# Performance work log

Hardware: AMD Instinct MI355X
Metric: run time of the kernel (lower is better)

The kernel has to match this reference:

```python
import jax, jax.numpy as jnp
import numpy as np

B, T, C = 2, 2048, 1024
NH = 16
HD = C // NH

def setup_inputs() -> dict:
    key = jax.random.key(0)
    k1, k2, k3 = jax.random.split(key, 3)
    x = jax.random.normal(k1, (B, T, C), dtype=jnp.float32)
    w_attn = jax.random.normal(k2, (C, 3 * C), dtype=jnp.float32) * 0.02
    w_proj = jax.random.normal(k3, (C, C), dtype=jnp.float32) * 0.02
    return {"x": x, "w_attn": w_attn, "w_proj": w_proj}

def reference(x, w_attn, w_proj):
    b, t, c = x.shape
    qkv = x @ w_attn                                  # [B,T,3C]
    q, k, v = jnp.split(qkv, 3, axis=-1)
    # [B,NH,T,HD]
    q = q.reshape(b, t, NH, HD).transpose(0, 2, 1, 3)
    k = k.reshape(b, t, NH, HD).transpose(0, 2, 1, 3)
    v = v.reshape(b, t, NH, HD).transpose(0, 2, 1, 3)
    scale = 1.0 / np.sqrt(HD).astype(np.float32)
    att = jnp.einsum('bhqd,bhkd->bhqk', q, k) * scale  # [B,NH,T,T]
    causal = jnp.tril(jnp.ones((t, t), dtype=bool))
    att = jnp.where(causal[None, None], att, jnp.float32(-jnp.inf))
    att = jax.nn.softmax(att, axis=-1)
    y = jnp.einsum('bhqk,bhkd->bhqd', att, v)          # [B,NH,T,HD]
    y = y.transpose(0, 2, 1, 3).reshape(b, t, c)
    return y @ w_proj
```

## Files before the change

kernel.cpp:

```cpp
#include <hip/hip_runtime.h>
#include <hip/hip_bf16.h>

#define BB 2
#define TT 2048
#define CCH 1024
#define NHH 16
#define HDD 64
#define M_TOK (BB*TT)
#define N_QKV (3*CCH)

typedef __attribute__((ext_vector_type(8))) short bf16x8;
typedef __attribute__((ext_vector_type(4))) float f32x4;
typedef unsigned short u16;
typedef unsigned int u32;

__device__ __forceinline__ u16 f2bf(float f) {
    union { float f; u32 u; } v; v.f = f;
    u32 u = v.u;
    u32 r = (u + 0x7FFFu + ((u >> 16) & 1u)) >> 16;
    return (u16)r;
}

__device__ __forceinline__ u32 pk_bf16(float a, float b) {
    u32 ua = __float_as_uint(a) + 0x8000u;
    u32 ub = __float_as_uint(b) + 0x8000u;
    return __builtin_amdgcn_perm(ub, ua, 0x07060302u);
}

__device__ __forceinline__ void async_copy16(const void* g, void* l) {
    __builtin_amdgcn_global_load_lds((__attribute__((address_space(1))) void*)g,
                                     (__attribute__((address_space(3))) void*)l,
                                     16, 0, 0);
}


__global__ __launch_bounds__(256) void cast_bf16_kernel(
    const float* __restrict__ src, u16* __restrict__ dst, int n4) {
    int i = blockIdx.x * 256 + threadIdx.x;
    if (i < n4) {
        float4 f = ((const float4*)src)[i];
        ushort4 o;
        o.x = f2bf(f.x); o.y = f2bf(f.y); o.z = f2bf(f.z); o.w = f2bf(f.w);
        ((ushort4*)dst)[i] = o;
    }
}

__global__ __launch_bounds__(256) void transpose_bf16_kernel(
    const float* __restrict__ src, u16* __restrict__ dst, int R, int Cn,
    int scale_rows, float sc) {
    __shared__ float tile[32][33];
    int c0 = blockIdx.x * 32, r0 = blockIdx.y * 32;
    int tx = threadIdx.x, ty = threadIdx.y;
#pragma unroll
    for (int i = ty; i < 32; i += 8)
        tile[i][tx] = src[(size_t)(r0 + i) * Cn + c0 + tx];
    __syncthreads();
#pragma unroll
    for (int i = ty; i < 32; i += 8) {
        float v = tile[tx][i];
        if (c0 + i < scale_rows) v *= sc;
        dst[(size_t)(c0 + i) * R + r0 + tx] = f2bf(v);
    }
}


template<int SWAP, int NJ>
__device__ __forceinline__ void gemm_kloop64(
    const u16* __restrict__ A, const u16* __restrict__ Bt, int K,
    int m0, int n0, int t, u16* __restrict__ As, u16* __restrict__ Bs,
    f32x4 (&acc)[4][4])
{
    int lane = t & 63, w = t >> 6;
    int mw = (w >> 1) * 64, nw = (w & 1) * (NJ * 16);
    int mr = lane & 15, quad = lane >> 4;
    int lr = lane >> 3;
    int cswz = (lane & 7) ^ lr;

    const u16* gA[4]; u16* lA[4];
#pragma unroll
    for (int p = 0; p < 4; ++p) {
        int grp = w * 4 + p;
        gA[p] = A + (size_t)(m0 + grp * 8 + lr) * K + cswz * 8;
        lA[p] = As + ((size_t)grp * 64 + lane) * 8;
    }
    const u16* gB[4]; u16* lB[4];
#pragma unroll
    for (int p = 0; p < NJ; ++p) {
        int grp = w * NJ + p;
        gB[p] = Bt + (size_t)(n0 + grp * 8 + lr) * K + cswz * 8;
        lB[p] = Bs + ((size_t)grp * 64 + lane) * 8;
    }

    int swm = mr & 7;
    for (int k0 = 0; k0 < K; k0 += 64) {
#pragma unroll
        for (int p = 0; p < 4; ++p) async_copy16(gA[p] + k0, lA[p]);
#pragma unroll
        for (int p = 0; p < NJ; ++p) async_copy16(gB[p] + k0, lB[p]);
        __syncthreads();
#pragma unroll
        for (int kk = 0; kk < 2; ++kk) {
            bf16x8 af[4], bfr[4];
#pragma unroll
            for (int i = 0; i < 4; ++i) {
                int r = mw + i * 16 + mr;
                af[i] = *(const bf16x8*)&As[r * 64 + (((kk * 4 + quad) ^ swm) << 3)];
            }
#pragma unroll
            for (int j = 0; j < NJ; ++j) {
                int r = nw + j * 16 + mr;
                bfr[j] = *(const bf16x8*)&Bs[r * 64 + (((kk * 4 + quad) ^ swm) << 3)];
            }
#pragma unroll
            for (int i = 0; i < 4; ++i)
#pragma unroll
                for (int j = 0; j < NJ; ++j) {
                    if (SWAP)
                        acc[i][j] = __builtin_amdgcn_mfma_f32_16x16x32_bf16(bfr[j], af[i], acc[i][j], 0, 0, 0);
                    else
                        acc[i][j] = __builtin_amdgcn_mfma_f32_16x16x32_bf16(af[i], bfr[j], acc[i][j], 0, 0, 0);
                }
        }
        __syncthreads();
    }
}


__global__ __launch_bounds__(256, 3) void qkv_gemm_kernel(
    const u16* __restrict__ A, const u16* __restrict__ Bt,
    u16* __restrict__ Qo, u16* __restrict__ Ko, u16* __restrict__ Vto)
{
    __shared__ u16 As[128 * 64];
    __shared__ u16 Bs[128 * 64];
    int t = threadIdx.x;
    int m0 = blockIdx.y * 128, n0 = blockIdx.x * 128;
    int part = n0 >> 10;
    int lane = t & 63, w = t >> 6;
    int mw = (w >> 1) * 64, nw = (w & 1) * 64;
    int mr = lane & 15, quad = lane >> 4;

    f32x4 zero = {0.f, 0.f, 0.f, 0.f};
    f32x4 acc[4][4];
#pragma unroll
    for (int i = 0; i < 4; ++i)
#pragma unroll
        for (int j = 0; j < 4; ++j) acc[i][j] = zero;

    if (part < 2) {
        gemm_kloop64<1, 4>(A, Bt, CCH, m0, n0, t, As, Bs, acc);
        u16* dstp = part ? Ko : Qo;
#pragma unroll
        for (int i = 0; i < 4; ++i)
#pragma unroll
            for (int j = 0; j < 4; ++j) {
                int tok = m0 + mw + i * 16 + mr;
                int cg0 = n0 + nw + j * 16 + quad * 4;
                int cc = cg0 & 1023;
                int h = cc >> 6, d0 = cc & 63;
                int b = tok >> 11, tt = tok & 2047;
                int bh = b * NHH + h;
                uint2 o;
                o.x = pk_bf16(acc[i][j][0], acc[i][j][1]);
                o.y = pk_bf16(acc[i][j][2], acc[i][j][3]);
                *(uint2*)&dstp[((size_t)bh * TT + tt) * HDD + d0] = o;
            }
    } else {
        gemm_kloop64<0, 4>(A, Bt, CCH, m0, n0, t, As, Bs, acc);
#pragma unroll
        for (int i = 0; i < 4; ++i)
#pragma unroll
            for (int j = 0; j < 4; ++j) {
                int t0 = m0 + mw + i * 16 + quad * 4;
                int cg = n0 + nw + j * 16 + mr;
                int cc = cg & 1023;
                int h = cc >> 6, d = cc & 63;
                int b = t0 >> 11, tt0 = t0 & 2047;
                int bh = b * NHH + h;
                uint2 o;
                o.x = pk_bf16(acc[i][j][0], acc[i][j][1]);
                o.y = pk_bf16(acc[i][j][2], acc[i][j][3]);
                *(uint2*)&Vto[((size_t)bh * HDD + d) * TT + tt0] = o;
            }
    }
}


__global__ __launch_bounds__(256) void proj_gemm_kernel(
    const u16* __restrict__ A, const u16* __restrict__ Bt, float* __restrict__ Cout)
{
    __shared__ u16 As[128 * 64];
    __shared__ u16 Bs[64 * 64];
    int t = threadIdx.x;
    int m0 = blockIdx.y * 128, n0 = blockIdx.x * 64;
    int lane = t & 63, w = t >> 6;
    int mw = (w >> 1) * 64, nw = (w & 1) * 32;
    int mr = lane & 15, quad = lane >> 4;

    f32x4 zero = {0.f, 0.f, 0.f, 0.f};
    f32x4 acc[4][4];
#pragma unroll
    for (int i = 0; i < 4; ++i)
#pragma unroll
        for (int j = 0; j < 4; ++j) acc[i][j] = zero;

    gemm_kloop64<1, 2>(A, Bt, CCH, m0, n0, t, As, Bs, acc);

#pragma unroll
    for (int i = 0; i < 4; ++i)
#pragma unroll
        for (int j = 0; j < 2; ++j) {
            int tok = m0 + mw + i * 16 + mr;
            int cg0 = n0 + nw + j * 16 + quad * 4;
            float4 v;
            v.x = acc[i][j][0]; v.y = acc[i][j][1];
            v.z = acc[i][j][2]; v.w = acc[i][j][3];
            *(float4*)&Cout[(size_t)tok * CCH + cg0] = v;
        }
}


#define PST2 40

template<bool MASK>
__device__ __forceinline__ void tile3(
    const u16* __restrict__ Kb, const u16* __restrict__ Vb, u16* __restrict__ pb,
    bf16x8 qf0, bf16x8 qf1, bf16x8 ones, int m, int quad, int sw, int kh,
    int kvb, int qcol, f32x4 (&o)[4], f32x4& lacc)
{
    f32x4 zero = {0.f, 0.f, 0.f, 0.f};
#pragma unroll
    for (int kc = 0; kc < 2; ++kc) {
        int rr = kh * 32 + kc * 16 + m;
        bf16x8 kf0 = *(const bf16x8*)&Kb[rr * 64 + ((quad ^ sw) << 3)];
        bf16x8 kf1 = *(const bf16x8*)&Kb[rr * 64 + (((quad + 4) ^ sw) << 3)];
        f32x4 s  = __builtin_amdgcn_mfma_f32_16x16x32_bf16(kf0, qf0, zero, 0, 0, 0);
        f32x4 st = __builtin_amdgcn_mfma_f32_16x16x32_bf16(kf1, qf1, s, 0, 0, 0);
        float e0, e1, e2, e3;
#pragma unroll
        for (int r = 0; r < 4; ++r) {
            float v = st[r];
            if (MASK && (kvb + kc * 16 + quad * 4 + r > qcol)) v = -1e30f;
            float e = __builtin_amdgcn_exp2f(v);
            if (r == 0) e0 = e; else if (r == 1) e1 = e; else if (r == 2) e2 = e; else e3 = e;
        }
        uint2 pk; pk.x = pk_bf16(e0, e1); pk.y = pk_bf16(e2, e3);
        *(uint2*)&pb[m * PST2 + kc * 16 + quad * 4] = pk;
    }
    bf16x8 pf = *(const bf16x8*)&pb[m * PST2 + quad * 8];
    lacc = __builtin_amdgcn_mfma_f32_16x16x32_bf16(ones, pf, lacc, 0, 0, 0);
#pragma unroll
    for (int dg = 0; dg < 4; ++dg) {
        int rr = dg * 16 + m;
        bf16x8 vf = *(const bf16x8*)&Vb[rr * 64 + (((kh * 4 + quad) ^ sw) << 3)];
        o[dg] = __builtin_amdgcn_mfma_f32_16x16x32_bf16(vf, pf, o[dg], 0, 0, 0);
    }
}

#define SM_U16 26880

__global__ __launch_bounds__(512, 2) void attn_kernel(
    const u16* __restrict__ Q, const u16* __restrict__ K,
    const u16* __restrict__ Vt, u16* __restrict__ Y)
{
    __shared__ __align__(16) u16 smem[SM_U16];
    int t = threadIdx.x;
    int w = t >> 6, lane = t & 63;
    int m = lane & 15, quad = lane >> 4;
    int iq = w >> 1, kh = w & 1;

    int bid = blockIdx.x;
    int head = bid & 31;
    int g = bid >> 5;
    int pr = (g < 8) ? g : 23 - g;
    int qbA = pr;
    int qbB = 31 - pr;
    int rbA = qbA * 64 + iq * 16;
    int rbB = qbB * 64 + iq * 16;

    const u16* qpA = Q + ((size_t)head * TT + rbA + m) * HDD + quad * 8;
    const u16* qpB = Q + ((size_t)head * TT + rbB + m) * HDD + quad * 8;
    bf16x8 qA0 = *(const bf16x8*)qpA;
    bf16x8 qA1 = *(const bf16x8*)(qpA + 32);
    bf16x8 qB0 = *(const bf16x8*)qpB;
    bf16x8 qB1 = *(const bf16x8*)(qpB + 32);

    bf16x8 ones;
#pragma unroll
    for (int i = 0; i < 8; ++i) ones[i] = (short)0x3F80;

    const u16* kbase = K + (size_t)head * TT * HDD;
    const u16* vbase = Vt + (size_t)head * HDD * TT;
    u16* pbA = smem + 16384 + (w * 2 + 0) * (16 * PST2);
    u16* pbB = smem + 16384 + (w * 2 + 1) * (16 * PST2);

    int lr = lane >> 3;
    int cg = (lane & 7) ^ lr;
    int r0 = w * 8 + lr;
    int loff = (w * 64 + lane) * 8;

    f32x4 zero = {0.f, 0.f, 0.f, 0.f};
    f32x4 oA[4], oB[4], laA = zero, laB = zero;
#pragma unroll
    for (int dg = 0; dg < 4; ++dg) { oA[dg] = zero; oB[dg] = zero; }
    int qcA = rbA + m, qcB = rbB + m;
    int sw = m & 7;

    async_copy16(kbase + (size_t)r0 * 64 + cg * 8, smem + loff);
    async_copy16(vbase + (size_t)r0 * TT + cg * 8, smem + 8192 + loff);

    for (int ic = 0; ic <= qbB; ++ic) {
        int buf = ic & 1;
        int kv0 = ic << 6;
        __syncthreads();
        if (ic < qbB) {
            int nkv = kv0 + 64;
            u16* dK = smem + (buf ^ 1) * 4096;
            u16* dV = smem + 8192 + (buf ^ 1) * 4096;
            async_copy16(kbase + (size_t)(nkv + r0) * 64 + cg * 8, dK + loff);
            async_copy16(vbase + (size_t)r0 * TT + nkv + cg * 8, dV + loff);
        }
        const u16* Kb = smem + buf * 4096;
        const u16* Vb = smem + 8192 + buf * 4096;
        int kvb = kv0 + kh * 32;
        if (ic < qbA)
            tile3<false>(Kb, Vb, pbA, qA0, qA1, ones, m, quad, sw, kh, kvb, qcA, oA, laA);
        else if (ic == qbA)
            tile3<true >(Kb, Vb, pbA, qA0, qA1, ones, m, quad, sw, kh, kvb, qcA, oA, laA);
        if (ic < qbB)
            tile3<false>(Kb, Vb, pbB, qB0, qB1, ones, m, quad, sw, kh, kvb, qcB, oB, laB);
        else
            tile3<true >(Kb, Vb, pbB, qB0, qB1, ones, m, quad, sw, kh, kvb, qcB, oB, laB);
    }

    float lA = laA[0];
    float lB = laB[0];

    __syncthreads();
    f32x4* ob = (f32x4*)smem;
    float* lb = (float*)&smem[26624];
    if (kh) {
        f32x4* dst = ob + (size_t)iq * 512 + lane;
#pragma unroll
        for (int dg = 0; dg < 4; ++dg) {
            dst[dg * 64] = oA[dg];
            dst[(4 + dg) * 64] = oB[dg];
        }
        if (quad == 0) {
            lb[(iq * 2 + 0) * 16 + m] = lA;
            lb[(iq * 2 + 1) * 16 + m] = lB;
        }
    }
    __syncthreads();
    if (!kh) {
        f32x4* src = ob + (size_t)iq * 512 + lane;
#pragma unroll
        for (int dg = 0; dg < 4; ++dg) {
            oA[dg] += src[dg * 64];
            oB[dg] += src[(4 + dg) * 64];
        }
        lA += lb[(iq * 2 + 0) * 16 + m];
        lB += lb[(iq * 2 + 1) * 16 + m];
        float invA = 1.0f / lA, invB = 1.0f / lB;

        int b = head >> 4, h = head & 15;
        size_t roA = ((size_t)(b * TT + rbA + m)) * CCH + h * HDD;
        size_t roB = ((size_t)(b * TT + rbB + m)) * CCH + h * HDD;
#pragma unroll
        for (int dg = 0; dg < 4; ++dg) {
            uint2 ov;
            ov.x = pk_bf16(oA[dg][0] * invA, oA[dg][1] * invA);
            ov.y = pk_bf16(oA[dg][2] * invA, oA[dg][3] * invA);
            *(uint2*)&Y[roA + dg * 16 + quad * 4] = ov;
            ov.x = pk_bf16(oB[dg][0] * invB, oB[dg][1] * invB);
            ov.y = pk_bf16(oB[dg][2] * invB, oB[dg][3] * invB);
            *(uint2*)&Y[roB + dg * 16 + quad * 4] = ov;
        }
    }
}


extern "C" void kernel_launch(void* const* d_in, const int* in_sizes, int n_in,
                              void* d_out, int out_size, void* d_ws, size_t ws_size,
                              hipStream_t stream) {
    const float* x      = (const float*)d_in[0];
    const float* w_attn = (const float*)d_in[1];
    const float* w_proj = (const float*)d_in[2];
    float* out = (float*)d_out;

    char* ws = (char*)d_ws;
    u16* x_bf   = (u16*)ws; ws += (size_t)M_TOK * CCH * 2;
    u16* wqkvT  = (u16*)ws; ws += (size_t)N_QKV * CCH * 2;
    u16* wprojT = (u16*)ws; ws += (size_t)CCH * CCH * 2;
    u16* qbuf   = (u16*)ws; ws += (size_t)BB * NHH * TT * HDD * 2;
    u16* kbuf   = (u16*)ws; ws += (size_t)BB * NHH * TT * HDD * 2;
    u16* vtb    = (u16*)ws; ws += (size_t)BB * NHH * HDD * TT * 2;
    u16* yb     = (u16*)ws; ws += (size_t)M_TOK * CCH * 2;

    const float QSC = 0.125f * 1.44269504088896f;

    cast_bf16_kernel<<<dim3(M_TOK * CCH / 4 / 256), dim3(256), 0, stream>>>(x, x_bf, M_TOK * CCH / 4);
    transpose_bf16_kernel<<<dim3(N_QKV / 32, CCH / 32), dim3(32, 8), 0, stream>>>(
        w_attn, wqkvT, CCH, N_QKV, CCH, QSC);
    transpose_bf16_kernel<<<dim3(CCH / 32, CCH / 32), dim3(32, 8), 0, stream>>>(
        w_proj, wprojT, CCH, CCH, 0, 1.0f);
    qkv_gemm_kernel<<<dim3(24, 32), dim3(256), 0, stream>>>(
        x_bf, wqkvT, qbuf, kbuf, vtb);
    attn_kernel<<<dim3(512), dim3(512), 0, stream>>>(qbuf, kbuf, vtb, yb);
    proj_gemm_kernel<<<dim3(16, 32), dim3(256), 0, stream>>>(yb, wprojT, out);
}
```

Measured before the change: 174.8 us.

## Rewrite QKV GEMM with 256x192 tiles and double-buffered async LDS pipeline

The QKV projection GEMM moves from 128x128 tiles with 256 threads to 256x192 tiles with 512 threads. Loads now go through a two-stage double-buffered async global-to-LDS pipeline with explicit waitcnt and barrier control, and the k-step is split in two halves so the next stage can be issued mid-iteration. The goal is to hide memory latency and cut redundant operand traffic through more reuse per block. In exchange, the grid shrinks to 256 blocks at one block per CU. The V-transpose epilogue now writes single scalar bf16 values with strided addressing, which may coalesce poorly.

```diff
diff --git a/kernel.cpp b/kernel.cpp
--- a/kernel.cpp
+++ b/kernel.cpp
@@ -126,62 +126,122 @@
 }
 
 
-__global__ __launch_bounds__(256, 3) void qkv_gemm_kernel(
+#define QKV_NK 16
+#define QKV_AS_HALF 16384
+#define QKV_BS_HALF 12288
+#define QKV_SMEM_BYTES ((2*QKV_AS_HALF + 2*QKV_BS_HALF) * 2)
+
+__global__ __launch_bounds__(512, 1) void qkv_gemm_kernel(
     const u16* __restrict__ A, const u16* __restrict__ Bt,
     u16* __restrict__ Qo, u16* __restrict__ Ko, u16* __restrict__ Vto)
 {
-    __shared__ u16 As[128 * 64];
-    __shared__ u16 Bs[128 * 64];
+    extern __shared__ __align__(16) u16 smem[];
+    u16* AsB = smem;
+    u16* BsB = smem + 2 * QKV_AS_HALF;
     int t = threadIdx.x;
-    int m0 = blockIdx.y * 128, n0 = blockIdx.x * 128;
-    int part = n0 >> 10;
     int lane = t & 63, w = t >> 6;
-    int mw = (w >> 1) * 64, nw = (w & 1) * 64;
-    int mr = lane & 15, quad = lane >> 4;
+    int m0 = blockIdx.y * 256, n0 = blockIdx.x * 192;
+    int mw = (w >> 1) * 64, nw = (w & 1) * 96;
+    int mr = lane & 15, quad = lane >> 4, swm = mr & 7;
 
     f32x4 zero = {0.f, 0.f, 0.f, 0.f};
-    f32x4 acc[4][4];
+    f32x4 acc[4][6];
 #pragma unroll
     for (int i = 0; i < 4; ++i)
 #pragma unroll
-        for (int j = 0; j < 4; ++j) acc[i][j] = zero;
-
-    if (part < 2) {
-        gemm_kloop64<1, 4>(A, Bt, CCH, m0, n0, t, As, Bs, acc);
-        u16* dstp = part ? Ko : Qo;
+        for (int j = 0; j < 6; ++j) acc[i][j] = zero;
+
+    int lr = lane >> 3;
+    int cswz = (lane & 7) ^ lr;
+    const u16* gA[4]; int lAo[4];
+#pragma unroll
+    for (int p = 0; p < 4; ++p) {
+        int grp = w * 4 + p;
+        gA[p] = A + (size_t)(m0 + grp * 8 + lr) * CCH + cswz * 8;
+        lAo[p] = (grp * 64 + lane) * 8;
+    }
+    const u16* gB[3]; int lBo[3];
+#pragma unroll
+    for (int p = 0; p < 3; ++p) {
+        int grp = w * 3 + p;
+        gB[p] = Bt + (size_t)(n0 + grp * 8 + lr) * CCH + cswz * 8;
+        lBo[p] = (grp * 64 + lane) * 8;
+    }
+
+#define QKV_STAGE(K0, BUF) do {                                               \
+    u16* dA_ = AsB + (BUF) * QKV_AS_HALF;                                     \
+    u16* dB_ = BsB + (BUF) * QKV_BS_HALF;                                     \
+    _Pragma("unroll") for (int p_ = 0; p_ < 4; ++p_)                          \
+        async_copy16(gA[p_] + (K0), dA_ + lAo[p_]);                           \
+    _Pragma("unroll") for (int p_ = 0; p_ < 3; ++p_)                          \
+        async_copy16(gB[p_] + (K0), dB_ + lBo[p_]);                           \
+  } while (0)
+
+    QKV_STAGE(0, 0);
+    QKV_STAGE(64, 1);
+
+    for (int k = 0; k < QKV_NK; ++k) {
+        int cur = k & 1;
+        if (k == QKV_NK - 1) asm volatile("s_waitcnt vmcnt(0)" ::: "memory");
+        else                 asm volatile("s_waitcnt vmcnt(7)" ::: "memory");
+        __builtin_amdgcn_s_barrier();
+        asm volatile("" ::: "memory");
+        const u16* Ac = AsB + cur * QKV_AS_HALF;
+        const u16* Bc = BsB + cur * QKV_BS_HALF;
+        bf16x8 a0[4], a1[4], b0[6], b1[6];
+#pragma unroll
+        for (int i = 0; i < 4; ++i) {
+            int r = (mw + i * 16 + mr) * 64;
+            a0[i] = *(const bf16x8*)&Ac[r + ((quad ^ swm) << 3)];
+            a1[i] = *(const bf16x8*)&Ac[r + (((quad + 4) ^ swm) << 3)];
+        }
+#pragma unroll
+        for (int j = 0; j < 6; ++j) {
+            int r = (nw + j * 16 + mr) * 64;
+            b0[j] = *(const bf16x8*)&Bc[r + ((quad ^ swm) << 3)];
+            b1[j] = *(const bf16x8*)&Bc[r + (((quad + 4) ^ swm) << 3)];
+        }
 #pragma unroll
         for (int i = 0; i < 4; ++i)
 #pragma unroll
-            for (int j = 0; j < 4; ++j) {
-                int tok = m0 + mw + i * 16 + mr;
-                int cg0 = n0 + nw + j * 16 + quad * 4;
-                int cc = cg0 & 1023;
-                int h = cc >> 6, d0 = cc & 63;
-                int b = tok >> 11, tt = tok & 2047;
-                int bh = b * NHH + h;
+            for (int j = 0; j < 6; ++j)
+                acc[i][j] = __builtin_amdgcn_mfma_f32_16x16x32_bf16(b0[j], a0[i], acc[i][j], 0, 0, 0);
+        asm volatile("s_waitcnt lgkmcnt(0)" ::: "memory");
+        __builtin_amdgcn_sched_barrier(0);
+        __builtin_amdgcn_s_barrier();
+        asm volatile("" ::: "memory");
+        if (k < QKV_NK - 2) QKV_STAGE((k + 2) * 64, cur);
+#pragma unroll
+        for (int i = 0; i < 4; ++i)
+#pragma unroll
+            for (int j = 0; j < 6; ++j)
+                acc[i][j] = __builtin_amdgcn_mfma_f32_16x16x32_bf16(b1[j], a1[i], acc[i][j], 0, 0, 0);
+    }
+#undef QKV_STAGE
+
+#pragma unroll
+    for (int i = 0; i < 4; ++i)
+#pragma unroll
+        for (int j = 0; j < 6; ++j) {
+            int tok = m0 + mw + i * 16 + mr;
+            int cg0 = n0 + nw + j * 16 + quad * 4;
+            int part = cg0 >> 10;
+            int cc = cg0 & 1023;
+            int h = cc >> 6, d0 = cc & 63;
+            int b = tok >> 11, tt = tok & 2047;
+            int bh = b * NHH + h;
+            if (part < 2) {
+                u16* dstp = part ? Ko : Qo;
                 uint2 o;
                 o.x = pk_bf16(acc[i][j][0], acc[i][j][1]);
                 o.y = pk_bf16(acc[i][j][2], acc[i][j][3]);
                 *(uint2*)&dstp[((size_t)bh * TT + tt) * HDD + d0] = o;
+            } else {
+#pragma unroll
+                for (int r = 0; r < 4; ++r)
+                    Vto[((size_t)bh * HDD + d0 + r) * TT + tt] = f2bf(acc[i][j][r]);
             }
-    } else {
-        gemm_kloop64<0, 4>(A, Bt, CCH, m0, n0, t, As, Bs, acc);
-#pragma unroll
-        for (int i = 0; i < 4; ++i)
-#pragma unroll
-            for (int j = 0; j < 4; ++j) {
-                int t0 = m0 + mw + i * 16 + quad * 4;
-                int cg = n0 + nw + j * 16 + mr;
-                int cc = cg & 1023;
-                int h = cc >> 6, d = cc & 63;
-                int b = t0 >> 11, tt0 = t0 & 2047;
-                int bh = b * NHH + h;
-                uint2 o;
-                o.x = pk_bf16(acc[i][j][0], acc[i][j][1]);
-                o.y = pk_bf16(acc[i][j][2], acc[i][j][3]);
-                *(uint2*)&Vto[((size_t)bh * HDD + d) * TT + tt0] = o;
-            }
-    }
+        }
 }
 
 
@@ -396,6 +456,14 @@
     u16* vtb    = (u16*)ws; ws += (size_t)BB * NHH * HDD * TT * 2;
     u16* yb     = (u16*)ws; ws += (size_t)M_TOK * CCH * 2;
 
+    static bool attr_done = false;
+    if (!attr_done) {
+        (void)hipFuncSetAttribute(reinterpret_cast<const void*>(qkv_gemm_kernel),
+                                  hipFuncAttributeMaxDynamicSharedMemorySize,
+                                  QKV_SMEM_BYTES);
+        attr_done = true;
+    }
+
     const float QSC = 0.125f * 1.44269504088896f;
 
     cast_bf16_kernel<<<dim3(M_TOK * CCH / 4 / 256), dim3(256), 0, stream>>>(x, x_bf, M_TOK * CCH / 4);
@@ -403,7 +471,7 @@
         w_attn, wqkvT, CCH, N_QKV, CCH, QSC);
     transpose_bf16_kernel<<<dim3(CCH / 32, CCH / 32), dim3(32, 8), 0, stream>>>(
         w_proj, wprojT, CCH, CCH, 0, 1.0f);
-    qkv_gemm_kernel<<<dim3(24, 32), dim3(256), 0, stream>>>(
+    qkv_gemm_kernel<<<dim3(16, 16), dim3(512), QKV_SMEM_BYTES, stream>>>(
         x_bf, wqkvT, qbuf, kbuf, vtb);
     attn_kernel<<<dim3(512), dim3(512), 0, stream>>>(qbuf, kbuf, vtb, yb);
     proj_gemm_kernel<<<dim3(16, 32), dim3(256), 0, stream>>>(yb, wprojT, out);
```

New measurement: 166.0 us. 1.05x faster.
